# Kernel optimization log

Hardware: AMD Instinct MI355X
Metric: run time of the kernel (lower is better)

Reference implementation:

```python
import jax, jax.numpy as jnp
import numpy as np

R_MAX = 5.0
NUM_BESSEL = 8
P_CUT = 5.0
AVG_NEIGH = 16.0
SQ3 = 1.7320508075688772


def poly_cutoff(r):
    # PolynomialCutoff with p=5
    u = r / R_MAX
    p = P_CUT
    f = 1.0 - (p + 1.0) * (p + 2.0) / 2.0 * u**5 + p * (p + 2.0) * u**6 - p * (p + 1.0) / 2.0 * u**7
    return f * (u < 1.0)


def bessel_damped(r, t):
    # BesselSinBasis with heat-kernel diffusion damping exp(-k_n^2 t)
    n = jnp.arange(1, NUM_BESSEL + 1, dtype=r.dtype)  # [8]
    k = n * jnp.pi / R_MAX
    pref = jnp.sqrt(2.0 / R_MAX)
    return pref * jnp.sin(k * r) / r * jnp.exp(-(k**2) * t)  # [E,8]


def switch_norm(x, w, b, mw, vw, rm, rv, eps=1e-5):
    # SwitchNorm1d, eval mode (BN stats = running buffers)
    mean_ln = x.mean(1, keepdims=True)
    var_ln = x.var(1, keepdims=True, ddof=1)
    mws = jax.nn.softmax(mw)
    vws = jax.nn.softmax(vw)
    mean = mws[0] * mean_ln + mws[1] * rm
    var = vws[0] * var_ln + vws[1] * rv
    return (x - mean) / jnp.sqrt(var + eps) * w + b


def setup_inputs() -> dict:
    key = jax.random.key(0)
    ks = jax.random.split(key, 16)
    N, E = 10000, 160000
    d = {}
    d["node_feats"] = jax.random.normal(ks[0], (N, 512), jnp.float32)
    d["edge_attrs"] = jax.random.normal(ks[1], (E, 4), jnp.float32)
    d["edge_lengths"] = jax.random.uniform(ks[2], (E, 1), jnp.float32, 0.5, 4.9)
    d["t"] = jax.random.uniform(ks[3], (E, 1), jnp.float32, 0.01, 1.0)
    d["lengths"] = d["edge_lengths"]
    d["edge_index"] = jax.random.randint(ks[4], (2, E), 0, N)
    g = lambda k, sh: jax.random.normal(k, sh, jnp.float32)
    d["W_scalar"] = g(ks[5], (128, 128))
    d["W_up0"] = g(ks[6], (128, 128))
    d["W_up1"] = g(ks[7], (128, 128))
    d["sn_weight"] = jnp.ones((1, 265), jnp.float32)
    d["sn_bias"] = jnp.zeros((1, 265), jnp.float32)
    d["sn_mean_w"] = jnp.ones((2,), jnp.float32)
    d["sn_var_w"] = jnp.ones((2,), jnp.float32)
    d["sn_run_mean"] = jnp.zeros((1, 265), jnp.float32)
    d["sn_run_var"] = jnp.zeros((1, 265), jnp.float32)
    d["W1"] = g(ks[8], (265, 64))
    d["W2"] = g(ks[9], (64, 64))
    d["W3"] = g(ks[10], (64, 64))
    d["W4"] = g(ks[11], (64, 512))
    d["W_out0"] = g(ks[12], (256, 128))
    d["W_out1"] = g(ks[13], (256, 128))
    return d


def reference(node_feats, edge_attrs, edge_lengths, t, lengths, edge_index,
              W_scalar, W_up0, W_up1,
              sn_weight, sn_bias, sn_mean_w, sn_var_w, sn_run_mean, sn_run_var,
              W1, W2, W3, W4, W_out0, W_out1):
    sender, receiver = edge_index[0], edge_index[1]
    N = node_feats.shape[0]
    s_in = node_feats[:, :128]                        # 0e block [N,128]
    v_in = node_feats[:, 128:].reshape(N, 128, 3)     # 1o block [N,128,3]
    inv = 1.0 / jnp.sqrt(128.0)                       # e3nn Linear fan-in norm
    node_scalars = s_in @ W_scalar * inv              # linear_scalar -> [N,128]
    s_up = s_in @ W_up0 * inv                         # linear_up (0e)
    v_up = jnp.einsum('nud,uo->nod', v_in, W_up1) * inv  # linear_up (1o)

    cutoff = poly_cutoff(edge_lengths)                # [E,1]
    emb = bessel_damped(edge_lengths, t) * cutoff     # radial_embedding [E,8]

    wi = jnp.concatenate([node_scalars[sender] * cutoff,
                          node_scalars[receiver] * cutoff,
                          emb,
                          lengths * cutoff], axis=-1)  # [E,265]
    wi = switch_norm(wi, sn_weight, sn_bias, sn_mean_w, sn_var_w, sn_run_mean, sn_run_var)

    # FullyConnectedNet [265,64,64,64,512], SiLU, fan-in normalized, no bias
    h = jax.nn.silu(wi @ W1 / jnp.sqrt(265.0))
    h = jax.nn.silu(h @ W2 / 8.0)
    h = jax.nn.silu(h @ W3 / 8.0)
    tpw = h @ W4 / 8.0                                 # [E,512]
    w0, w1, w2, w3 = tpw[:, :128], tpw[:, 128:256], tpw[:, 256:384], tpw[:, 384:]

    se = s_up[sender]                                  # [E,128]
    ve = v_up[sender]                                  # [E,128,3]
    y0 = edge_attrs[:, :1]                             # [E,1] (0e sh)
    y1 = edge_attrs[:, 1:4]                            # [E,3] (1o sh)

    # weighted uvu tensor product (CG contractions)
    out0a = w0 * se * y0                                        # 0e x 0e -> 0e
    out0b = w3 * jnp.einsum('eud,ed->eu', ve, y1) / SQ3         # 1o x 1o -> 0e
    out1a = (w1 * se)[:, :, None] * y1[:, None, :]              # 0e x 1o -> 1o
    out1b = w2[:, :, None] * ve * y0[:, None, :]                # 1o x 0e -> 1o

    m0 = jnp.concatenate([out0a, out0b], axis=-1)               # [E,256]
    m1 = jnp.concatenate([out1a, out1b], axis=1)                # [E,256,3]

    M0 = jax.ops.segment_sum(m0, receiver, num_segments=N)      # scatter_sum
    M1 = jax.ops.segment_sum(m1, receiver, num_segments=N)

    inv2 = 1.0 / jnp.sqrt(256.0)
    o0 = M0 @ W_out0 * (inv2 / AVG_NEIGH)                       # [N,128]
    o1 = jnp.einsum('nud,uo->nod', M1, W_out1) * (inv2 / AVG_NEIGH)  # [N,128,3]

    # reshape_irreps: [N, channels, 1+3]
    return jnp.concatenate([o0[:, :, None], o1], axis=2)
```

## Files before the change

### kernel.cpp

```cpp
#include <hip/hip_runtime.h>
#include <hip/hip_bf16.h>
#include <math.h>


#define PI_F 3.14159265358979323846f

typedef short  short8 __attribute__((ext_vector_type(8)));
typedef short  short4v __attribute__((ext_vector_type(4)));
typedef float  f32x4 __attribute__((ext_vector_type(4)));

static __device__ __forceinline__ float silu_f(float x) {
  return x / (1.0f + __expf(-x));
}
static __device__ __forceinline__ short f2bf(float x) {
  __hip_bfloat16 h = __float2bfloat16(x);
  return *reinterpret_cast<short*>(&h);
}
static __device__ __forceinline__ float bf2f(short s) {
  __hip_bfloat16 h = *reinterpret_cast<__hip_bfloat16*>(&s);
  return __bfloat162float(h);
}

__global__ __launch_bounds__(256)
void prep_weights(const float* __restrict__ W1, const float* __restrict__ W2,
                  const float* __restrict__ W3, const float* __restrict__ W4,
                  const float* __restrict__ Wsc, const float* __restrict__ Wu0,
                  const float* __restrict__ Wu1,
                  const float* __restrict__ Wo0, const float* __restrict__ Wo1,
                  short* __restrict__ frags)
{
  int t = blockIdx.x * 256 + threadIdx.x;
  if (t >= 340 * 64) return;
  int frag = t >> 6, lane = t & 63;
  const float* W; int K, Nout, kk, nt; float scale;
  if (frag < 36)       { int f = frag;       W = W1; K = 265; Nout = 64;  kk = f >> 2; nt = f & 3;  scale = 1.0f / sqrtf(265.0f); }
  else if (frag < 44)  { int f = frag - 36;  W = W2; K = 64;  Nout = 64;  kk = f >> 2; nt = f & 3;  scale = 0.125f; }
  else if (frag < 52)  { int f = frag - 44;  W = W3; K = 64;  Nout = 64;  kk = f >> 2; nt = f & 3;  scale = 0.125f; }
  else if (frag < 116) { int f = frag - 52;  W = W4; K = 64;  Nout = 512; kk = f >> 5; nt = f & 31;
                         scale = 0.125f * ((nt >= 24) ? 0.57735026918962576f : 1.0f); }
  else if (frag < 212) { int f = frag - 116; int m = f >> 5; kk = (f >> 3) & 3; nt = f & 7;
                         W = (m == 0) ? Wsc : ((m == 1) ? Wu0 : Wu1);
                         K = 128; Nout = 128; scale = 0.088388347648318447f; }
  else if (frag < 276) { int f = frag - 212; W = Wo0; K = 256; Nout = 128; kk = f >> 3; nt = f & 7;
                         scale = 1.0f / 256.0f; }
  else                 { int f = frag - 276; W = Wo1; K = 256; Nout = 128; kk = f >> 3; nt = f & 7;
                         scale = 1.0f / 256.0f; }
  int n = nt * 16 + (lane & 15);
  short* out = frags + ((size_t)(frag * 64 + lane)) * 8;
#pragma unroll
  for (int i = 0; i < 8; i++) {
    int k = kk * 32 + ((lane >> 4) << 3) + i;
    float v = (k < K) ? W[(size_t)k * Nout + n] * scale : 0.0f;
    out[i] = f2bf(v);
  }
}

#define NPW 16
__global__ __launch_bounds__(128)
void node_mfma(const float* __restrict__ nf, const short* __restrict__ frags,
               short* __restrict__ ns_bf, short4v* __restrict__ suvu, int N)
{
  __shared__ __align__(16) short sA[2][16][520];

  const int tid = threadIdx.x, lane = tid & 63, w = tid >> 6;
  const int nbase = blockIdx.x * (2 * NPW) + w * NPW;

  for (int it = 0; it < 32; ++it) {
    int idx = it * 64 + lane;
    int nd  = idx >> 7;
    int c4  = (idx & 127) << 2;
    int gn  = nbase + nd; if (gn >= N) gn = N - 1;
    float4 g = *(const float4*)&nf[(size_t)gn * 512 + c4];
#pragma unroll
    for (int i = 0; i < 4; i++) {
      int c = c4 + i;
      int pos;
      if (c < 128) pos = c;
      else { int j = c - 128; int u = j / 3, d = j - 3 * u; pos = 128 + (d << 7) + u; }
      sA[w][nd][pos] = f2bf(((const float*)&g)[i]);
    }
  }
  __syncthreads();

  const int arow = lane & 15;
  const int kgrp = (lane >> 4) << 3;
  short8 af[4][4];
#pragma unroll
  for (int m = 0; m < 4; m++)
#pragma unroll
    for (int kk = 0; kk < 4; kk++)
      af[m][kk] = *(const short8*)&sA[w][arow][m * 128 + kk * 32 + kgrp];

  const short8* F = (const short8*)frags;
#pragma unroll
  for (int nt = 0; nt < 8; ++nt) {
    f32x4 c_ns = {0,0,0,0}, c_su = {0,0,0,0};
    f32x4 c_vx = {0,0,0,0}, c_vy = {0,0,0,0}, c_vz = {0,0,0,0};
#pragma unroll
    for (int kk = 0; kk < 4; ++kk) {
      c_ns = __builtin_amdgcn_mfma_f32_16x16x32_bf16(af[0][kk], F[(116 + (0 * 4 + kk) * 8 + nt) * 64 + lane], c_ns, 0, 0, 0);
      c_su = __builtin_amdgcn_mfma_f32_16x16x32_bf16(af[0][kk], F[(116 + (1 * 4 + kk) * 8 + nt) * 64 + lane], c_su, 0, 0, 0);
      c_vx = __builtin_amdgcn_mfma_f32_16x16x32_bf16(af[1][kk], F[(116 + (2 * 4 + kk) * 8 + nt) * 64 + lane], c_vx, 0, 0, 0);
      c_vy = __builtin_amdgcn_mfma_f32_16x16x32_bf16(af[2][kk], F[(116 + (2 * 4 + kk) * 8 + nt) * 64 + lane], c_vy, 0, 0, 0);
      c_vz = __builtin_amdgcn_mfma_f32_16x16x32_bf16(af[3][kk], F[(116 + (2 * 4 + kk) * 8 + nt) * 64 + lane], c_vz, 0, 0, 0);
    }
    const int col = nt * 16 + (lane & 15);
#pragma unroll
    for (int rr = 0; rr < 4; ++rr) {
      int nd = nbase + ((lane >> 4) << 2) + rr;
      if (nd < N) {
        ns_bf[(size_t)nd * 128 + col] = f2bf(c_ns[rr]);
        short4v p;
        p[0] = f2bf(c_su[rr]); p[1] = f2bf(c_vx[rr]);
        p[2] = f2bf(c_vy[rr]); p[3] = f2bf(c_vz[rr]);
        suvu[(size_t)nd * 128 + col] = p;
      }
    }
  }
}

__global__ __launch_bounds__(256)
void prep_norm(const float* __restrict__ snw, const float* __restrict__ snb,
               const float* __restrict__ snmw, const float* __restrict__ snvw,
               const float* __restrict__ snrm, const float* __restrict__ snrv,
               float4* __restrict__ nrm_c)
{
  int k = blockIdx.x * 256 + threadIdx.x;
  float msm0 = 1.0f / (1.0f + __expf(snmw[1] - snmw[0]));
  float vsm0 = 1.0f / (1.0f + __expf(snvw[1] - snvw[0]));
  if (k < 265) {
    float4 c;
    c.x = (1.0f - msm0) * snrm[k];
    c.y = (1.0f - vsm0) * snrv[k] + 1e-5f;
    c.z = snw[k];
    c.w = snb[k];
    nrm_c[k] = c;
  } else if (k == 265) {
    float4 c; c.x = msm0; c.y = vsm0; c.z = 0.f; c.w = 0.f;
    nrm_c[k] = c;
  }
}

__global__ __launch_bounds__(256)
void hist_kernel(const int* __restrict__ eidx, int* __restrict__ cnt, int E)
{
  int e = blockIdx.x * 256 + threadIdx.x;
  if (e < E) atomicAdd(&cnt[eidx[E + e]], 1);
}

__global__ __launch_bounds__(1024)
void scan_kernel(const int* __restrict__ cnt, int* __restrict__ rs,
                 int* __restrict__ cursor, int N)
{
  __shared__ int wsum[16];
  __shared__ int carry_s;
  const int tid = threadIdx.x, lane = tid & 63, wid = tid >> 6;
  if (tid == 0) { carry_s = 0; rs[0] = 0; }
  __syncthreads();
  for (int base = 0; base < N; base += 1024) {
    int i = base + tid;
    int v = (i < N) ? cnt[i] : 0;
    int x = v;
#pragma unroll
    for (int off = 1; off < 64; off <<= 1) {
      int t = __shfl_up(x, off);
      if (lane >= off) x += t;
    }
    if (lane == 63) wsum[wid] = x;
    __syncthreads();
    if (tid == 0) {
      int acc = carry_s;
#pragma unroll
      for (int k = 0; k < 16; k++) { int t = wsum[k]; wsum[k] = acc; acc += t; }
      carry_s = acc;
    }
    __syncthreads();
    int inc = x + wsum[wid];
    if (i < N) { rs[i + 1] = inc; cursor[i] = inc - v; }
    __syncthreads();
  }
}

__global__ __launch_bounds__(256)
void scatter_kernel(const int* __restrict__ eidx, int* __restrict__ cursor,
                    int* __restrict__ perm, int E)
{
  int e = blockIdx.x * 256 + threadIdx.x;
  if (e < E) {
    int r = eidx[E + e];
    int pos = atomicAdd(&cursor[r], 1);
    perm[pos] = e;
  }
}

#define EB 32

__global__ __launch_bounds__(128, 4)
void edge_mlp(const float* __restrict__ elen,
              const float* __restrict__ tdif,
              const float* __restrict__ lens,
              const int*   __restrict__ eidx,
              const float4* __restrict__ nrm_c,
              const short* __restrict__ ns_bf,
              const short* __restrict__ frags,
              const int*   __restrict__ perm,
              short* __restrict__ tpw,
              int e_lo, int E)
{
  __shared__ __align__(16) float smu[288], sva[288], sw_[288], sb_[288];
  __shared__ __align__(16) short hA[EB][72];
  __shared__ __align__(16) short hB[EB][72];

  const int tid  = threadIdx.x;
  const int lane = tid & 63;
  const int w    = tid >> 6;

  for (int i = tid; i < 288; i += 128) {
    float4 c;
    if (i < 265) c = nrm_c[i];
    else { c.x = 0.f; c.y = 1.f; c.z = 0.f; c.w = 0.f; }
    smu[i] = c.x; sva[i] = c.y; sw_[i] = c.z; sb_[i] = c.w;
  }
  const float4 mix = nrm_c[265];
  const float msm0 = mix.x, vsm0 = mix.y;

  const int e16 = lane & 15, grp = lane >> 4;
  int gi = e_lo + blockIdx.x * EB + w * 16 + e16;
  if (gi >= E) gi = E - 1;
  const int e = perm[gi];
  const int snd = eidx[e], rcv = eidx[E + e];
  const float r = elen[e], tt = tdif[e];
  float uu_ = r * 0.2f;
  float u2 = uu_ * uu_, u4 = u2 * u2, u5 = u4 * uu_;
  float cc = 1.0f - 21.0f * u5 + 35.0f * u5 * uu_ - 15.0f * u5 * u2;
  const float cut = (uu_ < 1.0f) ? cc : 0.0f;
  const float lncut = lens[e] * cut;

  short8 raw[9];
  float s1 = 0.f, s2 = 0.f;
#pragma unroll
  for (int kk = 0; kk < 9; ++kk) {
    float v[8];
    if (kk < 4) {
      short8 g = *(const short8*)&ns_bf[(size_t)snd * 128 + kk * 32 + grp * 8];
#pragma unroll
      for (int i = 0; i < 8; i++) v[i] = bf2f(g[i]) * cut;
    } else if (kk < 8) {
      short8 g = *(const short8*)&ns_bf[(size_t)rcv * 128 + (kk - 4) * 32 + grp * 8];
#pragma unroll
      for (int i = 0; i < 8; i++) v[i] = bf2f(g[i]) * cut;
    } else {
      if (grp == 0) {
        const float pref = sqrtf(0.4f);
#pragma unroll
        for (int i = 0; i < 8; i++) {
          float kn = (float)(i + 1) * (PI_F / 5.0f);
          v[i] = pref * __sinf(kn * r) / r * __expf(-kn * kn * tt) * cut;
        }
      } else if (grp == 1) {
        v[0] = lncut;
#pragma unroll
        for (int i = 1; i < 8; i++) v[i] = 0.f;
      } else {
#pragma unroll
        for (int i = 0; i < 8; i++) v[i] = 0.f;
      }
    }
#pragma unroll
    for (int i = 0; i < 8; i++) {
      s1 += v[i]; s2 += v[i] * v[i];
      raw[kk][i] = f2bf(v[i]);
    }
  }
  s1 += __shfl_xor(s1, 16); s1 += __shfl_xor(s1, 32);
  s2 += __shfl_xor(s2, 16); s2 += __shfl_xor(s2, 32);
  const float mean = s1 * (1.0f / 265.0f);
  const float var  = (s2 - s1 * mean) * (1.0f / 264.0f);
  const float mupart = msm0 * mean;
  const float vapart = vsm0 * var;

  __syncthreads();

  const short8* F = (const short8*)frags;
  const int arow = w * 16 + (lane & 15);
  const int kgrp = (lane >> 4) << 3;

  f32x4 A0 = {0,0,0,0}, A1 = {0,0,0,0}, A2 = {0,0,0,0}, A3 = {0,0,0,0};
#pragma unroll
  for (int kk = 0; kk < 9; ++kk) {
    const int k0 = kk * 32 + grp * 8;
    short8 a;
#pragma unroll
    for (int h = 0; h < 2; ++h) {
      float4 mu4 = *(const float4*)&smu[k0 + 4 * h];
      float4 va4 = *(const float4*)&sva[k0 + 4 * h];
      float4 w4  = *(const float4*)&sw_[k0 + 4 * h];
      float4 b4  = *(const float4*)&sb_[k0 + 4 * h];
#pragma unroll
      for (int i = 0; i < 4; ++i) {
        float x  = bf2f(raw[kk][4 * h + i]);
        float mu = mupart + ((const float*)&mu4)[i];
        float va = vapart + ((const float*)&va4)[i];
        a[4 * h + i] = f2bf(fmaf((x - mu) * rsqrtf(va), ((const float*)&w4)[i], ((const float*)&b4)[i]));
      }
    }
    A0 = __builtin_amdgcn_mfma_f32_16x16x32_bf16(a, F[(kk * 4 + 0) * 64 + lane], A0, 0, 0, 0);
    A1 = __builtin_amdgcn_mfma_f32_16x16x32_bf16(a, F[(kk * 4 + 1) * 64 + lane], A1, 0, 0, 0);
    A2 = __builtin_amdgcn_mfma_f32_16x16x32_bf16(a, F[(kk * 4 + 2) * 64 + lane], A2, 0, 0, 0);
    A3 = __builtin_amdgcn_mfma_f32_16x16x32_bf16(a, F[(kk * 4 + 3) * 64 + lane], A3, 0, 0, 0);
  }
#pragma unroll
  for (int rr = 0; rr < 4; ++rr) {
    int er = w * 16 + ((lane >> 4) << 2) + rr;
    hA[er][ 0 + (lane & 15)] = f2bf(silu_f(A0[rr]));
    hA[er][16 + (lane & 15)] = f2bf(silu_f(A1[rr]));
    hA[er][32 + (lane & 15)] = f2bf(silu_f(A2[rr]));
    hA[er][48 + (lane & 15)] = f2bf(silu_f(A3[rr]));
  }
  __syncthreads();

  A0 = A1 = A2 = A3 = (f32x4){0,0,0,0};
#pragma unroll
  for (int kk = 0; kk < 2; ++kk) {
    short8 a = *(const short8*)&hA[arow][kk * 32 + kgrp];
    A0 = __builtin_amdgcn_mfma_f32_16x16x32_bf16(a, F[(36 + kk * 4 + 0) * 64 + lane], A0, 0, 0, 0);
    A1 = __builtin_amdgcn_mfma_f32_16x16x32_bf16(a, F[(36 + kk * 4 + 1) * 64 + lane], A1, 0, 0, 0);
    A2 = __builtin_amdgcn_mfma_f32_16x16x32_bf16(a, F[(36 + kk * 4 + 2) * 64 + lane], A2, 0, 0, 0);
    A3 = __builtin_amdgcn_mfma_f32_16x16x32_bf16(a, F[(36 + kk * 4 + 3) * 64 + lane], A3, 0, 0, 0);
  }
#pragma unroll
  for (int rr = 0; rr < 4; ++rr) {
    int er = w * 16 + ((lane >> 4) << 2) + rr;
    hB[er][ 0 + (lane & 15)] = f2bf(silu_f(A0[rr]));
    hB[er][16 + (lane & 15)] = f2bf(silu_f(A1[rr]));
    hB[er][32 + (lane & 15)] = f2bf(silu_f(A2[rr]));
    hB[er][48 + (lane & 15)] = f2bf(silu_f(A3[rr]));
  }
  __syncthreads();

  A0 = A1 = A2 = A3 = (f32x4){0,0,0,0};
#pragma unroll
  for (int kk = 0; kk < 2; ++kk) {
    short8 a = *(const short8*)&hB[arow][kk * 32 + kgrp];
    A0 = __builtin_amdgcn_mfma_f32_16x16x32_bf16(a, F[(44 + kk * 4 + 0) * 64 + lane], A0, 0, 0, 0);
    A1 = __builtin_amdgcn_mfma_f32_16x16x32_bf16(a, F[(44 + kk * 4 + 1) * 64 + lane], A1, 0, 0, 0);
    A2 = __builtin_amdgcn_mfma_f32_16x16x32_bf16(a, F[(44 + kk * 4 + 2) * 64 + lane], A2, 0, 0, 0);
    A3 = __builtin_amdgcn_mfma_f32_16x16x32_bf16(a, F[(44 + kk * 4 + 3) * 64 + lane], A3, 0, 0, 0);
  }
  __syncthreads();
#pragma unroll
  for (int rr = 0; rr < 4; ++rr) {
    int er = w * 16 + ((lane >> 4) << 2) + rr;
    hA[er][ 0 + (lane & 15)] = f2bf(silu_f(A0[rr]));
    hA[er][16 + (lane & 15)] = f2bf(silu_f(A1[rr]));
    hA[er][32 + (lane & 15)] = f2bf(silu_f(A2[rr]));
    hA[er][48 + (lane & 15)] = f2bf(silu_f(A3[rr]));
  }
  __syncthreads();

  short8 a40 = *(const short8*)&hA[arow][ 0 + kgrp];
  short8 a41 = *(const short8*)&hA[arow][32 + kgrp];
  const int rowbase = blockIdx.x * EB + w * 16 + ((lane >> 4) << 2);

#pragma unroll
  for (int t = 0; t < 8; ++t) {
    f32x4 W0 = {0,0,0,0}, W1t = {0,0,0,0}, W2t = {0,0,0,0}, W3t = {0,0,0,0};
    W0  = __builtin_amdgcn_mfma_f32_16x16x32_bf16(a40, F[(52 + 0 * 32 + ( 0 + t)) * 64 + lane], W0,  0, 0, 0);
    W0  = __builtin_amdgcn_mfma_f32_16x16x32_bf16(a41, F[(52 + 1 * 32 + ( 0 + t)) * 64 + lane], W0,  0, 0, 0);
    W1t = __builtin_amdgcn_mfma_f32_16x16x32_bf16(a40, F[(52 + 0 * 32 + ( 8 + t)) * 64 + lane], W1t, 0, 0, 0);
    W1t = __builtin_amdgcn_mfma_f32_16x16x32_bf16(a41, F[(52 + 1 * 32 + ( 8 + t)) * 64 + lane], W1t, 0, 0, 0);
    W2t = __builtin_amdgcn_mfma_f32_16x16x32_bf16(a40, F[(52 + 0 * 32 + (16 + t)) * 64 + lane], W2t, 0, 0, 0);
    W2t = __builtin_amdgcn_mfma_f32_16x16x32_bf16(a41, F[(52 + 1 * 32 + (16 + t)) * 64 + lane], W2t, 0, 0, 0);
    W3t = __builtin_amdgcn_mfma_f32_16x16x32_bf16(a40, F[(52 + 0 * 32 + (24 + t)) * 64 + lane], W3t, 0, 0, 0);
    W3t = __builtin_amdgcn_mfma_f32_16x16x32_bf16(a41, F[(52 + 1 * 32 + (24 + t)) * 64 + lane], W3t, 0, 0, 0);

    const int uu = t * 16 + (lane & 15);
#pragma unroll
    for (int rr = 0; rr < 4; ++rr) {
      short4v pk;
      pk[0] = f2bf(W0[rr]); pk[1] = f2bf(W1t[rr]);
      pk[2] = f2bf(W2t[rr]); pk[3] = f2bf(W3t[rr]);
      *(short4v*)(tpw + (size_t)(rowbase + rr) * 512 + uu * 4) = pk;
    }
  }
}

__global__ __launch_bounds__(128)
void gather_kernel(const int* __restrict__ rs, const int* __restrict__ perm,
                   const int* __restrict__ eidx, const float* __restrict__ eattr,
                   const short4v* __restrict__ suvu,
                   const short* __restrict__ tpw,
                   float* __restrict__ M0, float* __restrict__ M1,
                   int e_lo, int e_hi, int E, int writemode)
{
  __shared__ int   s_snd[64];
  __shared__ __align__(16) float s_y[64][4];

  const int n = blockIdx.x;
  const int o = threadIdx.x;
  int lo = rs[n], hi = rs[n + 1];
  if (lo < e_lo) lo = e_lo;
  if (hi > e_hi) hi = e_hi;
  if (!writemode && lo >= hi) return;

  float a0 = 0.f, a1 = 0.f;
  float b0 = 0.f, b1 = 0.f, b2 = 0.f;
  float c0 = 0.f, c1 = 0.f, c2 = 0.f;

  for (int base = lo; base < hi; base += 64) {
    const int cnt = min(64, hi - base);
    __syncthreads();
    if (o < cnt) {
      int e = perm[base + o];
      s_snd[o] = eidx[e];
      *(float4*)&s_y[o][0] = *(const float4*)&eattr[e * 4];
    }
    __syncthreads();
    for (int j = 0; j < cnt; ++j) {
      const int snd = s_snd[j];
      const float4 y = *(const float4*)&s_y[j][0];
      const short4v sv = suvu[(size_t)snd * 128 + o];
      short4v pk = *(const short4v*)(tpw + (size_t)(base + j - e_lo) * 512 + o * 4);
      const float se = bf2f(sv[0]);
      const float v0 = bf2f(sv[1]);
      const float v1 = bf2f(sv[2]);
      const float v2 = bf2f(sv[3]);
      const float w0 = bf2f(pk[0]), w1 = bf2f(pk[1]);
      const float w2 = bf2f(pk[2]), w3 = bf2f(pk[3]);
      const float dot = v0 * y.y + v1 * y.z + v2 * y.w;
      a0 = fmaf(w0 * se, y.x, a0);
      a1 = fmaf(w3, dot, a1);
      const float s1v = w1 * se;
      b0 = fmaf(s1v, y.y, b0); b1 = fmaf(s1v, y.z, b1); b2 = fmaf(s1v, y.w, b2);
      const float vv = w2 * y.x;
      c0 = fmaf(vv, v0, c0); c1 = fmaf(vv, v1, c1); c2 = fmaf(vv, v2, c2);
    }
  }
  float* p0 = M0 + (size_t)n * 256;
  float* p1 = M1 + (size_t)n * 3 * 256;
  if (writemode) {
    p0[o] = a0; p0[128 + o] = a1;
    p1[0 * 256 + o] = b0; p1[1 * 256 + o] = b1; p1[2 * 256 + o] = b2;
    p1[0 * 256 + 128 + o] = c0; p1[1 * 256 + 128 + o] = c1; p1[2 * 256 + 128 + o] = c2;
  } else {
    p0[o] += a0; p0[128 + o] += a1;
    p1[0 * 256 + o] += b0; p1[1 * 256 + o] += b1; p1[2 * 256 + o] += b2;
    p1[0 * 256 + 128 + o] += c0; p1[1 * 256 + 128 + o] += c1; p1[2 * 256 + 128 + o] += c2;
  }
}

__global__ __launch_bounds__(128)
void out_mfma(const float* __restrict__ M0, const float* __restrict__ M1,
              const short* __restrict__ frags, float* __restrict__ out, int N)
{
  const int tid = threadIdx.x, lane = tid & 63, w = tid >> 6;
  const int nbase = blockIdx.x * 32 + w * 16;
  const int kgrp = (lane >> 4) << 3;
  int nd = nbase + (lane & 15); if (nd >= N) nd = N - 1;

  const float* rowp[4];
  rowp[0] = M0 + (size_t)nd * 256;
  rowp[1] = M1 + ((size_t)nd * 3 + 0) * 256;
  rowp[2] = M1 + ((size_t)nd * 3 + 1) * 256;
  rowp[3] = M1 + ((size_t)nd * 3 + 2) * 256;

  f32x4 acc[8][4];
#pragma unroll
  for (int nt = 0; nt < 8; ++nt)
#pragma unroll
    for (int s = 0; s < 4; ++s) acc[nt][s] = (f32x4){0,0,0,0};

  const short8* F = (const short8*)frags;
#pragma unroll
  for (int kc = 0; kc < 8; ++kc) {
    short8 a[4];
#pragma unroll
    for (int s = 0; s < 4; ++s) {
      float4 g0 = *(const float4*)&rowp[s][kc * 32 + kgrp];
      float4 g1 = *(const float4*)&rowp[s][kc * 32 + kgrp + 4];
      short8 t;
      t[0] = f2bf(g0.x); t[1] = f2bf(g0.y); t[2] = f2bf(g0.z); t[3] = f2bf(g0.w);
      t[4] = f2bf(g1.x); t[5] = f2bf(g1.y); t[6] = f2bf(g1.z); t[7] = f2bf(g1.w);
      a[s] = t;
    }
#pragma unroll
    for (int nt = 0; nt < 8; ++nt) {
      short8 b0 = F[(212 + kc * 8 + nt) * 64 + lane];
      short8 b1 = F[(276 + kc * 8 + nt) * 64 + lane];
      acc[nt][0] = __builtin_amdgcn_mfma_f32_16x16x32_bf16(a[0], b0, acc[nt][0], 0, 0, 0);
      acc[nt][1] = __builtin_amdgcn_mfma_f32_16x16x32_bf16(a[1], b1, acc[nt][1], 0, 0, 0);
      acc[nt][2] = __builtin_amdgcn_mfma_f32_16x16x32_bf16(a[2], b1, acc[nt][2], 0, 0, 0);
      acc[nt][3] = __builtin_amdgcn_mfma_f32_16x16x32_bf16(a[3], b1, acc[nt][3], 0, 0, 0);
    }
  }

#pragma unroll
  for (int nt = 0; nt < 8; ++nt) {
    const int col = nt * 16 + (lane & 15);
#pragma unroll
    for (int rr = 0; rr < 4; ++rr) {
      int n = nbase + ((lane >> 4) << 2) + rr;
      if (n < N) {
        float4 r;
        r.x = acc[nt][0][rr];
        r.y = acc[nt][1][rr];
        r.z = acc[nt][2][rr];
        r.w = acc[nt][3][rr];
        *(float4*)(out + ((size_t)n * 128 + col) * 4) = r;
      }
    }
  }
}

extern "C" void kernel_launch(void* const* d_in, const int* in_sizes, int n_in,
                              void* d_out, int out_size, void* d_ws, size_t ws_size,
                              hipStream_t stream)
{
  const float* nf   = (const float*)d_in[0];
  const float* eattr= (const float*)d_in[1];
  const float* elen = (const float*)d_in[2];
  const float* tdif = (const float*)d_in[3];
  const float* lens = (const float*)d_in[4];
  const int*   eidx = (const int*)  d_in[5];
  const float* Wsc  = (const float*)d_in[6];
  const float* Wu0  = (const float*)d_in[7];
  const float* Wu1  = (const float*)d_in[8];
  const float* snw  = (const float*)d_in[9];
  const float* snb  = (const float*)d_in[10];
  const float* snmw = (const float*)d_in[11];
  const float* snvw = (const float*)d_in[12];
  const float* snrm = (const float*)d_in[13];
  const float* snrv = (const float*)d_in[14];
  const float* W1   = (const float*)d_in[15];
  const float* W2   = (const float*)d_in[16];
  const float* W3   = (const float*)d_in[17];
  const float* W4   = (const float*)d_in[18];
  const float* Wo0  = (const float*)d_in[19];
  const float* Wo1  = (const float*)d_in[20];

  const int N = in_sizes[0] / 512;
  const int E = in_sizes[1] / 4;

  char* p = (char*)d_ws;
  short*   ns_bf = (short*)p;    p += (size_t)N * 128 * 2;
  short4v* suvu  = (short4v*)p;  p += (size_t)N * 128 * 8;
  float*   M0    = (float*)p;    p += (size_t)N * 256 * 4;
  float*   M1    = (float*)p;    p += (size_t)N * 768 * 4;
  float4*  nrm_c = (float4*)p;   p += 266 * 16;
  short*   frags = (short*)p;    p += (size_t)340 * 64 * 8 * 2;
  int* cnt    = (int*)p;         p += (size_t)N * 4;
  int* rs     = (int*)p;         p += (size_t)(N + 1) * 4;
  int* cursor = (int*)p;         p += (size_t)N * 4;
  int* perm   = (int*)p;         p += (size_t)E * 4;
  size_t used = (size_t)(p - (char*)d_ws);
  used = (used + 255) & ~(size_t)255;
  short* tpw = (short*)((char*)d_ws + used);
  size_t avail = (ws_size > used) ? (ws_size - used) : 0;

  long long chunk = (long long)(avail / 1024) & ~31LL;
  long long Eup = ((long long)E + 31) & ~31LL;
  if (chunk > Eup) chunk = Eup;
  if (chunk < 32)  chunk = 32;
  const int writemode = (chunk >= Eup) ? 1 : 0;

  if (!writemode)
    hipMemsetAsync(M0, 0, (size_t)1024 * N * sizeof(float), stream);
  hipMemsetAsync(cnt, 0, (size_t)N * sizeof(int), stream);

  prep_weights<<<dim3((340 * 64 + 255) / 256), dim3(256), 0, stream>>>(
      W1, W2, W3, W4, Wsc, Wu0, Wu1, Wo0, Wo1, frags);
  prep_norm<<<dim3(2), dim3(256), 0, stream>>>(snw, snb, snmw, snvw, snrm, snrv, nrm_c);
  node_mfma<<<dim3((N + 31) / 32), dim3(128), 0, stream>>>(nf, frags, ns_bf, suvu, N);
  hist_kernel<<<dim3((E + 255) / 256), dim3(256), 0, stream>>>(eidx, cnt, E);
  scan_kernel<<<dim3(1), dim3(1024), 0, stream>>>(cnt, rs, cursor, N);
  scatter_kernel<<<dim3((E + 255) / 256), dim3(256), 0, stream>>>(eidx, cursor, perm, E);

  for (long long lo = 0; lo < E; lo += chunk) {
    int n_e = (int)(((long long)E - lo < chunk) ? ((long long)E - lo) : chunk);
    int blocks = (n_e + EB - 1) / EB;
    edge_mlp<<<dim3(blocks), dim3(128), 0, stream>>>(
        elen, tdif, lens, eidx, nrm_c, ns_bf, frags, perm, tpw, (int)lo, E);
    gather_kernel<<<dim3(N), dim3(128), 0, stream>>>(
        rs, perm, eidx, eattr, suvu, tpw, M0, M1, (int)lo, (int)(lo + n_e), E, writemode);
  }

  out_mfma<<<dim3((N + 31) / 32), dim3(128), 0, stream>>>(M0, M1, frags, (float*)d_out, N);
}
```

Measured before the change: 229.1 us.

## Fuse edge MLP with receiver-sorted segmented scatter and merge prep kernels

```diff
diff --git a/kernel.cpp b/kernel.cpp
--- a/kernel.cpp
+++ b/kernel.cpp
@@ -22,36 +22,62 @@
 }
 
 __global__ __launch_bounds__(256)
-void prep_weights(const float* __restrict__ W1, const float* __restrict__ W2,
-                  const float* __restrict__ W3, const float* __restrict__ W4,
-                  const float* __restrict__ Wsc, const float* __restrict__ Wu0,
-                  const float* __restrict__ Wu1,
-                  const float* __restrict__ Wo0, const float* __restrict__ Wo1,
-                  short* __restrict__ frags)
-{
-  int t = blockIdx.x * 256 + threadIdx.x;
-  if (t >= 340 * 64) return;
-  int frag = t >> 6, lane = t & 63;
-  const float* W; int K, Nout, kk, nt; float scale;
-  if (frag < 36)       { int f = frag;       W = W1; K = 265; Nout = 64;  kk = f >> 2; nt = f & 3;  scale = 1.0f / sqrtf(265.0f); }
-  else if (frag < 44)  { int f = frag - 36;  W = W2; K = 64;  Nout = 64;  kk = f >> 2; nt = f & 3;  scale = 0.125f; }
-  else if (frag < 52)  { int f = frag - 44;  W = W3; K = 64;  Nout = 64;  kk = f >> 2; nt = f & 3;  scale = 0.125f; }
-  else if (frag < 116) { int f = frag - 52;  W = W4; K = 64;  Nout = 512; kk = f >> 5; nt = f & 31;
-                         scale = 0.125f * ((nt >= 24) ? 0.57735026918962576f : 1.0f); }
-  else if (frag < 212) { int f = frag - 116; int m = f >> 5; kk = (f >> 3) & 3; nt = f & 7;
-                         W = (m == 0) ? Wsc : ((m == 1) ? Wu0 : Wu1);
-                         K = 128; Nout = 128; scale = 0.088388347648318447f; }
-  else if (frag < 276) { int f = frag - 212; W = Wo0; K = 256; Nout = 128; kk = f >> 3; nt = f & 7;
-                         scale = 1.0f / 256.0f; }
-  else                 { int f = frag - 276; W = Wo1; K = 256; Nout = 128; kk = f >> 3; nt = f & 7;
-                         scale = 1.0f / 256.0f; }
-  int n = nt * 16 + (lane & 15);
-  short* out = frags + ((size_t)(frag * 64 + lane)) * 8;
-#pragma unroll
-  for (int i = 0; i < 8; i++) {
-    int k = kk * 32 + ((lane >> 4) << 3) + i;
-    float v = (k < K) ? W[(size_t)k * Nout + n] * scale : 0.0f;
-    out[i] = f2bf(v);
+void prep_fused(const float* __restrict__ W1, const float* __restrict__ W2,
+                const float* __restrict__ W3, const float* __restrict__ W4,
+                const float* __restrict__ Wsc, const float* __restrict__ Wu0,
+                const float* __restrict__ Wu1,
+                const float* __restrict__ Wo0, const float* __restrict__ Wo1,
+                const float* __restrict__ snw, const float* __restrict__ snb,
+                const float* __restrict__ snmw, const float* __restrict__ snvw,
+                const float* __restrict__ snrm, const float* __restrict__ snrv,
+                const int* __restrict__ eidx,
+                short* __restrict__ frags, float4* __restrict__ nrm_c,
+                int* __restrict__ cnt, int E)
+{
+  const int b = blockIdx.x;
+  if (b < 85) {
+    int t = b * 256 + threadIdx.x;
+    if (t >= 340 * 64) return;
+    int frag = t >> 6, lane = t & 63;
+    const float* W; int K, Nout, kk, nt; float scale;
+    if (frag < 36)       { int f = frag;       W = W1; K = 265; Nout = 64;  kk = f >> 2; nt = f & 3;  scale = 1.0f / sqrtf(265.0f); }
+    else if (frag < 44)  { int f = frag - 36;  W = W2; K = 64;  Nout = 64;  kk = f >> 2; nt = f & 3;  scale = 0.125f; }
+    else if (frag < 52)  { int f = frag - 44;  W = W3; K = 64;  Nout = 64;  kk = f >> 2; nt = f & 3;  scale = 0.125f; }
+    else if (frag < 116) { int f = frag - 52;  W = W4; K = 64;  Nout = 512; kk = f >> 5; nt = f & 31;
+                           scale = 0.125f * ((nt >= 24) ? 0.57735026918962576f : 1.0f); }
+    else if (frag < 212) { int f = frag - 116; int m = f >> 5; kk = (f >> 3) & 3; nt = f & 7;
+                           W = (m == 0) ? Wsc : ((m == 1) ? Wu0 : Wu1);
+                           K = 128; Nout = 128; scale = 0.088388347648318447f; }
+    else if (frag < 276) { int f = frag - 212; W = Wo0; K = 256; Nout = 128; kk = f >> 3; nt = f & 7;
+                           scale = 1.0f / 256.0f; }
+    else                 { int f = frag - 276; W = Wo1; K = 256; Nout = 128; kk = f >> 3; nt = f & 7;
+                           scale = 1.0f / 256.0f; }
+    int n = nt * 16 + (lane & 15);
+    short* out = frags + ((size_t)(frag * 64 + lane)) * 8;
+#pragma unroll
+    for (int i = 0; i < 8; i++) {
+      int k = kk * 32 + ((lane >> 4) << 3) + i;
+      float v = (k < K) ? W[(size_t)k * Nout + n] * scale : 0.0f;
+      out[i] = f2bf(v);
+    }
+  } else if (b < 87) {
+    int k = (b - 85) * 256 + threadIdx.x;
+    float msm0 = 1.0f / (1.0f + __expf(snmw[1] - snmw[0]));
+    float vsm0 = 1.0f / (1.0f + __expf(snvw[1] - snvw[0]));
+    if (k < 265) {
+      float4 c;
+      c.x = (1.0f - msm0) * snrm[k];
+      c.y = (1.0f - vsm0) * snrv[k] + 1e-5f;
+      c.z = snw[k];
+      c.w = snb[k];
+      nrm_c[k] = c;
+    } else if (k == 265) {
+      float4 c; c.x = msm0; c.y = vsm0; c.z = 0.f; c.w = 0.f;
+      nrm_c[k] = c;
+    }
+  } else {
+    int e = (b - 87) * 256 + threadIdx.x;
+    if (e < E) atomicAdd(&cnt[eidx[E + e]], 1);
   }
 }
 
@@ -119,35 +145,6 @@
   }
 }
 
-__global__ __launch_bounds__(256)
-void prep_norm(const float* __restrict__ snw, const float* __restrict__ snb,
-               const float* __restrict__ snmw, const float* __restrict__ snvw,
-               const float* __restrict__ snrm, const float* __restrict__ snrv,
-               float4* __restrict__ nrm_c)
-{
-  int k = blockIdx.x * 256 + threadIdx.x;
-  float msm0 = 1.0f / (1.0f + __expf(snmw[1] - snmw[0]));
-  float vsm0 = 1.0f / (1.0f + __expf(snvw[1] - snvw[0]));
-  if (k < 265) {
-    float4 c;
-    c.x = (1.0f - msm0) * snrm[k];
-    c.y = (1.0f - vsm0) * snrv[k] + 1e-5f;
-    c.z = snw[k];
-    c.w = snb[k];
-    nrm_c[k] = c;
-  } else if (k == 265) {
-    float4 c; c.x = msm0; c.y = vsm0; c.z = 0.f; c.w = 0.f;
-    nrm_c[k] = c;
-  }
-}
-
-__global__ __launch_bounds__(256)
-void hist_kernel(const int* __restrict__ eidx, int* __restrict__ cnt, int E)
-{
-  int e = blockIdx.x * 256 + threadIdx.x;
-  if (e < E) atomicAdd(&cnt[eidx[E + e]], 1);
-}
-
 __global__ __launch_bounds__(1024)
 void scan_kernel(const int* __restrict__ cnt, int* __restrict__ rs,
                  int* __restrict__ cursor, int N)
@@ -196,20 +193,30 @@
 #define EB 32
 
 __global__ __launch_bounds__(128, 4)
-void edge_mlp(const float* __restrict__ elen,
-              const float* __restrict__ tdif,
-              const float* __restrict__ lens,
-              const int*   __restrict__ eidx,
-              const float4* __restrict__ nrm_c,
-              const short* __restrict__ ns_bf,
-              const short* __restrict__ frags,
-              const int*   __restrict__ perm,
-              short* __restrict__ tpw,
-              int e_lo, int E)
-{
-  __shared__ __align__(16) float smu[288], sva[288], sw_[288], sb_[288];
+void edge_fused(const float* __restrict__ elen,
+                const float* __restrict__ tdif,
+                const float* __restrict__ lens,
+                const int*   __restrict__ eidx,
+                const float* __restrict__ eattr,
+                const float4* __restrict__ nrm_c,
+                const short* __restrict__ ns_bf,
+                const short4v* __restrict__ suvu,
+                const short* __restrict__ frags,
+                const int*   __restrict__ perm,
+                const int*   __restrict__ rs,
+                float* __restrict__ M0, float* __restrict__ M1,
+                int E)
+{
+  __shared__ __align__(16) char arena[33280];
+  float* smu = (float*)(arena + 0);
+  float* sva = (float*)(arena + 1152);
+  float* sw_ = (float*)(arena + 2304);
+  float* sb_ = (float*)(arena + 3456);
+  short (*hB)[72]   = (short(*)[72])(arena + 4608);
+  short (*tpwl)[520]= (short(*)[520])(arena);
   __shared__ __align__(16) short hA[EB][72];
-  __shared__ __align__(16) short hB[EB][72];
+  __shared__ int s_snd[EB], s_rcv[EB];
+  __shared__ __align__(16) float s_y[EB][4];
 
   const int tid  = threadIdx.x;
   const int lane = tid & 63;
@@ -225,10 +232,17 @@
   const float msm0 = mix.x, vsm0 = mix.y;
 
   const int e16 = lane & 15, grp = lane >> 4;
-  int gi = e_lo + blockIdx.x * EB + w * 16 + e16;
-  if (gi >= E) gi = E - 1;
+  const int el  = w * 16 + e16;
+  int gi = blockIdx.x * EB + el;
+  const bool validE = (gi < E);
+  if (!validE) gi = E - 1;
   const int e = perm[gi];
   const int snd = eidx[e], rcv = eidx[E + e];
+  if (grp == 0) {
+    s_snd[el] = snd; s_rcv[el] = rcv;
+    float4 yv = validE ? *(const float4*)&eattr[e * 4] : (float4){0.f, 0.f, 0.f, 0.f};
+    *(float4*)&s_y[el][0] = yv;
+  }
   const float r = elen[e], tt = tdif[e];
   float uu_ = r * 0.2f;
   float u2 = uu_ * uu_, u4 = u2 * u2, u5 = u4 * uu_;
@@ -301,7 +315,8 @@
         float x  = bf2f(raw[kk][4 * h + i]);
         float mu = mupart + ((const float*)&mu4)[i];
         float va = vapart + ((const float*)&va4)[i];
-        a[4 * h + i] = f2bf(fmaf((x - mu) * rsqrtf(va), ((const float*)&w4)[i], ((const float*)&b4)[i]));
+        float rsq = __builtin_amdgcn_rsq(va);
+        a[4 * h + i] = f2bf(fmaf((x - mu) * rsq, ((const float*)&w4)[i], ((const float*)&b4)[i]));
       }
     }
     A0 = __builtin_amdgcn_mfma_f32_16x16x32_bf16(a, F[(kk * 4 + 0) * 64 + lane], A0, 0, 0, 0);
@@ -360,8 +375,9 @@
 
   short8 a40 = *(const short8*)&hA[arow][ 0 + kgrp];
   short8 a41 = *(const short8*)&hA[arow][32 + kgrp];
-  const int rowbase = blockIdx.x * EB + w * 16 + ((lane >> 4) << 2);
-
+  __syncthreads();
+
+  const int rowloc = w * 16 + ((lane >> 4) << 2);
 #pragma unroll
   for (int t = 0; t < 8; ++t) {
     f32x4 W0 = {0,0,0,0}, W1t = {0,0,0,0}, W2t = {0,0,0,0}, W3t = {0,0,0,0};
@@ -380,73 +396,64 @@
       short4v pk;
       pk[0] = f2bf(W0[rr]); pk[1] = f2bf(W1t[rr]);
       pk[2] = f2bf(W2t[rr]); pk[3] = f2bf(W3t[rr]);
-      *(short4v*)(tpw + (size_t)(rowbase + rr) * 512 + uu * 4) = pk;
-    }
-  }
-}
-
-__global__ __launch_bounds__(128)
-void gather_kernel(const int* __restrict__ rs, const int* __restrict__ perm,
-                   const int* __restrict__ eidx, const float* __restrict__ eattr,
-                   const short4v* __restrict__ suvu,
-                   const short* __restrict__ tpw,
-                   float* __restrict__ M0, float* __restrict__ M1,
-                   int e_lo, int e_hi, int E, int writemode)
-{
-  __shared__ int   s_snd[64];
-  __shared__ __align__(16) float s_y[64][4];
-
-  const int n = blockIdx.x;
-  const int o = threadIdx.x;
-  int lo = rs[n], hi = rs[n + 1];
-  if (lo < e_lo) lo = e_lo;
-  if (hi > e_hi) hi = e_hi;
-  if (!writemode && lo >= hi) return;
-
+      *(short4v*)&tpwl[rowloc + rr][uu * 4] = pk;
+    }
+  }
+  __syncthreads();
+
+  const int o = tid;
+  const int gbase = blockIdx.x * EB;
   float a0 = 0.f, a1 = 0.f;
   float b0 = 0.f, b1 = 0.f, b2 = 0.f;
   float c0 = 0.f, c1 = 0.f, c2 = 0.f;
-
-  for (int base = lo; base < hi; base += 64) {
-    const int cnt = min(64, hi - base);
-    __syncthreads();
-    if (o < cnt) {
-      int e = perm[base + o];
-      s_snd[o] = eidx[e];
-      *(float4*)&s_y[o][0] = *(const float4*)&eattr[e * 4];
-    }
-    __syncthreads();
-    for (int j = 0; j < cnt; ++j) {
-      const int snd = s_snd[j];
-      const float4 y = *(const float4*)&s_y[j][0];
-      const short4v sv = suvu[(size_t)snd * 128 + o];
-      short4v pk = *(const short4v*)(tpw + (size_t)(base + j - e_lo) * 512 + o * 4);
-      const float se = bf2f(sv[0]);
-      const float v0 = bf2f(sv[1]);
-      const float v1 = bf2f(sv[2]);
-      const float v2 = bf2f(sv[3]);
-      const float w0 = bf2f(pk[0]), w1 = bf2f(pk[1]);
-      const float w2 = bf2f(pk[2]), w3 = bf2f(pk[3]);
-      const float dot = v0 * y.y + v1 * y.z + v2 * y.w;
-      a0 = fmaf(w0 * se, y.x, a0);
-      a1 = fmaf(w3, dot, a1);
-      const float s1v = w1 * se;
-      b0 = fmaf(s1v, y.y, b0); b1 = fmaf(s1v, y.z, b1); b2 = fmaf(s1v, y.w, b2);
-      const float vv = w2 * y.x;
-      c0 = fmaf(vv, v0, c0); c1 = fmaf(vv, v1, c1); c2 = fmaf(vv, v2, c2);
-    }
-  }
-  float* p0 = M0 + (size_t)n * 256;
-  float* p1 = M1 + (size_t)n * 3 * 256;
-  if (writemode) {
-    p0[o] = a0; p0[128 + o] = a1;
-    p1[0 * 256 + o] = b0; p1[1 * 256 + o] = b1; p1[2 * 256 + o] = b2;
-    p1[0 * 256 + 128 + o] = c0; p1[1 * 256 + 128 + o] = c1; p1[2 * 256 + 128 + o] = c2;
-  } else {
-    p0[o] += a0; p0[128 + o] += a1;
-    p1[0 * 256 + o] += b0; p1[1 * 256 + o] += b1; p1[2 * 256 + o] += b2;
-    p1[0 * 256 + 128 + o] += c0; p1[1 * 256 + 128 + o] += c1; p1[2 * 256 + 128 + o] += c2;
-  }
+  int cur = s_rcv[0];
+  int segstart = gbase;
+
+#define FLUSH(nID, gs, ge) do { \
+    const int n_ = (nID); \
+    float* p0 = M0 + (size_t)n_ * 256; \
+    float* p1 = M1 + (size_t)n_ * 768; \
+    if (rs[n_] == (gs) && rs[n_ + 1] == (ge)) { \
+      p0[o] = a0; p0[128 + o] = a1; \
+      p1[o] = b0; p1[256 + o] = b1; p1[512 + o] = b2; \
+      p1[128 + o] = c0; p1[384 + o] = c1; p1[640 + o] = c2; \
+    } else { \
+      atomicAdd(&p0[o], a0); atomicAdd(&p0[128 + o], a1); \
+      atomicAdd(&p1[o], b0); atomicAdd(&p1[256 + o], b1); atomicAdd(&p1[512 + o], b2); \
+      atomicAdd(&p1[128 + o], c0); atomicAdd(&p1[384 + o], c1); atomicAdd(&p1[640 + o], c2); \
+    } \
+  } while (0)
+
+  for (int j = 0; j < EB; ++j) {
+    const int rj = s_rcv[j];
+    if (rj != cur) {
+      FLUSH(cur, segstart, gbase + j);
+      a0 = a1 = b0 = b1 = b2 = c0 = c1 = c2 = 0.f;
+      cur = rj; segstart = gbase + j;
+    }
+    const int sndj = s_snd[j];
+    const float4 y = *(const float4*)&s_y[j][0];
+    const short4v sv = suvu[(size_t)sndj * 128 + o];
+    const short4v pk = *(const short4v*)&tpwl[j][o * 4];
+    const float se = bf2f(sv[0]);
+    const float v0 = bf2f(sv[1]);
+    const float v1 = bf2f(sv[2]);
+    const float v2 = bf2f(sv[3]);
+    const float w0 = bf2f(pk[0]), w1 = bf2f(pk[1]);
+    const float w2 = bf2f(pk[2]), w3 = bf2f(pk[3]);
+    const float dot = v0 * y.y + v1 * y.z + v2 * y.w;
+    a0 = fmaf(w0 * se, y.x, a0);
+    a1 = fmaf(w3, dot, a1);
+    const float s1v = w1 * se;
+    b0 = fmaf(s1v, y.y, b0); b1 = fmaf(s1v, y.z, b1); b2 = fmaf(s1v, y.w, b2);
+    const float vv = w2 * y.x;
+    c0 = fmaf(vv, v0, c0); c1 = fmaf(vv, v1, c1); c2 = fmaf(vv, v2, c2);
+  }
+  {
+    int ge = gbase + EB; if (ge > E) ge = E;
+    FLUSH(cur, segstart, ge);
+  }
+#undef FLUSH
 }
 
 __global__ __launch_bounds__(128)
@@ -460,9 +467,9 @@
 
   const float* rowp[4];
   rowp[0] = M0 + (size_t)nd * 256;
-  rowp[1] = M1 + ((size_t)nd * 3 + 0) * 256;
-  rowp[2] = M1 + ((size_t)nd * 3 + 1) * 256;
-  rowp[3] = M1 + ((size_t)nd * 3 + 2) * 256;
+  rowp[1] = M1 + (size_t)nd * 768;
+  rowp[2] = M1 + (size_t)nd * 768 + 256;
+  rowp[3] = M1 + (size_t)nd * 768 + 512;
 
   f32x4 acc[8][4];
 #pragma unroll
@@ -552,37 +559,20 @@
   int* rs     = (int*)p;         p += (size_t)(N + 1) * 4;
   int* cursor = (int*)p;         p += (size_t)N * 4;
   int* perm   = (int*)p;         p += (size_t)E * 4;
-  size_t used = (size_t)(p - (char*)d_ws);
-  used = (used + 255) & ~(size_t)255;
-  short* tpw = (short*)((char*)d_ws + used);
-  size_t avail = (ws_size > used) ? (ws_size - used) : 0;
-
-  long long chunk = (long long)(avail / 1024) & ~31LL;
-  long long Eup = ((long long)E + 31) & ~31LL;
-  if (chunk > Eup) chunk = Eup;
-  if (chunk < 32)  chunk = 32;
-  const int writemode = (chunk >= Eup) ? 1 : 0;
-
-  if (!writemode)
-    hipMemsetAsync(M0, 0, (size_t)1024 * N * sizeof(float), stream);
+
+  hipMemsetAsync(M0, 0, (size_t)1024 * N * sizeof(float), stream);
   hipMemsetAsync(cnt, 0, (size_t)N * sizeof(int), stream);
 
-  prep_weights<<<dim3((340 * 64 + 255) / 256), dim3(256), 0, stream>>>(
-      W1, W2, W3, W4, Wsc, Wu0, Wu1, Wo0, Wo1, frags);
-  prep_norm<<<dim3(2), dim3(256), 0, stream>>>(snw, snb, snmw, snvw, snrm, snrv, nrm_c);
+  const int hist_blocks = (E + 255) / 256;
+  prep_fused<<<dim3(87 + hist_blocks), dim3(256), 0, stream>>>(
+      W1, W2, W3, W4, Wsc, Wu0, Wu1, Wo0, Wo1,
+      snw, snb, snmw, snvw, snrm, snrv, eidx, frags, nrm_c, cnt, E);
   node_mfma<<<dim3((N + 31) / 32), dim3(128), 0, stream>>>(nf, frags, ns_bf, suvu, N);
-  hist_kernel<<<dim3((E + 255) / 256), dim3(256), 0, stream>>>(eidx, cnt, E);
   scan_kernel<<<dim3(1), dim3(1024), 0, stream>>>(cnt, rs, cursor, N);
   scatter_kernel<<<dim3((E + 255) / 256), dim3(256), 0, stream>>>(eidx, cursor, perm, E);
 
-  for (long long lo = 0; lo < E; lo += chunk) {
-    int n_e = (int)(((long long)E - lo < chunk) ? ((long long)E - lo) : chunk);
-    int blocks = (n_e + EB - 1) / EB;
-    edge_mlp<<<dim3(blocks), dim3(128), 0, stream>>>(
-        elen, tdif, lens, eidx, nrm_c, ns_bf, frags, perm, tpw, (int)lo, E);
-    gather_kernel<<<dim3(N), dim3(128), 0, stream>>>(
-        rs, perm, eidx, eattr, suvu, tpw, M0, M1, (int)lo, (int)(lo + n_e), E, writemode);
-  }
+  edge_fused<<<dim3((E + EB - 1) / EB), dim3(128), 0, stream>>>(
+      elen, tdif, lens, eidx, eattr, nrm_c, ns_bf, suvu, frags, perm, rs, M0, M1, E);
 
   out_mfma<<<dim3((N + 31) / 32), dim3(128), 0, stream>>>(M0, M1, frags, (float*)d_out, N);
 }
```

Result: slower. 258.1 us (+12.7%).
